# Kernel optimization log

Hardware: AMD Instinct MI355X
Metric: run time of the kernel (lower is better)

The kernel has to match this reference:

```python
import jax, jax.numpy as jnp
import numpy as np

N_NODES = 100000
N_EDGES = 3200000
IN_F, HID_F, OUT_F = 128, 128, 64
BN_EPS = 1e-5


def setup_inputs() -> dict:
    key = jax.random.key(0)
    ks = jax.random.split(key, 12)
    x = jax.random.normal(ks[0], (N_NODES, IN_F), dtype=jnp.float32)
    src = jax.random.randint(ks[1], (N_EDGES,), 0, N_NODES, dtype=jnp.int64)
    dst = jax.random.randint(ks[2], (N_EDGES,), 0, N_NODES, dtype=jnp.int64)
    s = 0.05
    W1 = jax.random.normal(ks[3], (IN_F, HID_F), dtype=jnp.float32) * s
    b1 = jnp.zeros((HID_F,), jnp.float32)
    W2 = jax.random.normal(ks[4], (HID_F, HID_F), dtype=jnp.float32) * s
    b2 = jnp.zeros((HID_F,), jnp.float32)
    W3 = jax.random.normal(ks[5], (HID_F, OUT_F), dtype=jnp.float32) * s
    b3 = jnp.zeros((OUT_F,), jnp.float32)
    gamma1 = jnp.ones((HID_F,), jnp.float32)
    beta1 = jnp.zeros((HID_F,), jnp.float32)
    gamma2 = jnp.ones((HID_F,), jnp.float32)
    beta2 = jnp.zeros((HID_F,), jnp.float32)
    return {"x": x, "src": src, "dst": dst,
            "W1": W1, "b1": b1, "W2": W2, "b2": b2, "W3": W3, "b3": b3,
            "gamma1": gamma1, "beta1": beta1, "gamma2": gamma2, "beta2": beta2}


def reference(x, src, dst, W1, b1, W2, b2, W3, b3, gamma1, beta1, gamma2, beta2):
    n = x.shape[0]
    ones = jnp.ones((src.shape[0],), x.dtype)
    # DGL GraphConv(norm='both'): symmetric normalization, degrees clamped to >=1
    deg_out = jax.ops.segment_sum(ones, src, num_segments=n)
    deg_in = jax.ops.segment_sum(ones, dst, num_segments=n)
    norm_s = jax.lax.rsqrt(jnp.maximum(deg_out, 1.0))[:, None]
    norm_d = jax.lax.rsqrt(jnp.maximum(deg_in, 1.0))[:, None]

    def conv(h, W, b):
        h = h * norm_s                                   # [N, F] scale by out-deg^{-1/2}
        m = jax.ops.segment_sum(h[src], dst, num_segments=n)  # SpMM aggregation
        return (m * norm_d) @ W + b

    def bn(h, g, b):  # BatchNorm1d, training-mode batch stats (biased var)
        mu = jnp.mean(h, axis=0)
        var = jnp.var(h, axis=0)
        return (h - mu) * jax.lax.rsqrt(var + BN_EPS) * g + b

    h = bn(jax.nn.relu(conv(x, W1, b1)), gamma1, beta1)
    h = bn(jax.nn.relu(conv(h, W2, b2)), gamma2, beta2)
    h = conv(h, W3, b3)
    return jax.nn.log_softmax(h, axis=1)
```

## Files before the change

kernel.cpp:

```cpp
#include <hip/hip_runtime.h>
#include <hip/hip_bf16.h>
#include <cstdint>

static constexpr int N = 100000;
static constexpr int E = 3200000;
static constexpr float BN_EPS = 1e-5f;
static constexpr int NBUCK = (N + 127) >> 7;
static constexpr int NBLK = 256;
static constexpr int CHUNK = E / NBLK;
static constexpr int AGG_BLOCKS = 2048;
static constexpr int NWAVE = AGG_BLOCKS * 4;

static constexpr size_t OFF_TOT_D = 0;
static constexpr size_t OFF_TOT_S = 3328;
static constexpr size_t OFF_DBASE = 6656;
static constexpr size_t OFF_SBASE = 9984;
static constexpr size_t OFF_AB1   = 13312;
static constexpr size_t OFF_AB2   = 14336;
static constexpr size_t OFF_CVEC  = 15360;
static constexpr size_t OFF_WT    = 16384;
static constexpr size_t OFF_WSRT  = 49152;
static constexpr size_t OFF_BNP2  = 82944;
static constexpr size_t OFF_BNP   = 148480;
static constexpr size_t OFF_NORM_S= 2245632;
static constexpr size_t OFF_NORM_D= 2645632;
static constexpr size_t OFF_RP    = 3045632;
static constexpr size_t OFF_CNT_D = 3445760;
static constexpr size_t OFF_CNT_S = 4246528;
static constexpr size_t OFF_OFFD  = 5047296;
static constexpr size_t OFF_OFFS  = 5848064;
static constexpr size_t OFF_COL   = 6648832;
static constexpr size_t OFF_SRCB  = 19448832;
static constexpr size_t OFF_PAIRS = 22648832;
static constexpr size_t OFF_H     = 35448832;
static constexpr size_t OFF_T     = 61048832;

using short8  = __attribute__((ext_vector_type(8))) short;
using float4v = __attribute__((ext_vector_type(4))) float;

__device__ inline float bflo(unsigned v) { return __uint_as_float(v << 16); }
__device__ inline float bfhi(unsigned v) { return __uint_as_float(v & 0xffff0000u); }
__device__ inline unsigned short bfbits(float x) {
    __hip_bfloat16 h = __float2bfloat16(x);
    return *reinterpret_cast<unsigned short*>(&h);
}

__global__ __launch_bounds__(256) void k_count(const int* __restrict__ src,
                                               const int* __restrict__ dst,
                                               int* __restrict__ cnt_s,
                                               int* __restrict__ cnt_d) {
    __shared__ int hs[NBUCK], hd[NBUCK];
    int tid = threadIdx.x, blk = blockIdx.x;
    for (int b = tid; b < NBUCK; b += 256) { hs[b] = 0; hd[b] = 0; }
    __syncthreads();
    int e0 = blk * CHUNK, e1 = min(E, e0 + CHUNK);
    for (int e = e0 + tid; e < e1; e += 256) {
        atomicAdd(&hs[src[e] >> 7], 1);
        atomicAdd(&hd[dst[e] >> 7], 1);
    }
    __syncthreads();
    for (int b = tid; b < NBUCK; b += 256) {
        cnt_s[blk * NBUCK + b] = hs[b];
        cnt_d[blk * NBUCK + b] = hd[b];
    }
}

__global__ __launch_bounds__(256) void k_scanA(const int* __restrict__ cnt,
                                               int* __restrict__ off,
                                               int* __restrict__ tot) {
    __shared__ int sd[256];
    int b = blockIdx.x, tid = threadIdx.x;
    int v = cnt[tid * NBUCK + b];
    sd[tid] = v;
    __syncthreads();
    for (int o = 1; o < 256; o <<= 1) {
        int t = (tid >= o) ? sd[tid - o] : 0;
        __syncthreads();
        sd[tid] += t;
        __syncthreads();
    }
    off[tid * NBUCK + b] = sd[tid] - v;
    if (tid == 255) tot[b] = sd[255];
}

__global__ __launch_bounds__(1024) void k_scanB(const int* __restrict__ tot_d,
                                                const int* __restrict__ tot_s,
                                                int* __restrict__ dbase,
                                                int* __restrict__ sbase) {
    __shared__ int sd[1024], ss[1024];
    int tid = threadIdx.x;
    int vd = (tid < NBUCK) ? tot_d[tid] : 0;
    int vs = (tid < NBUCK) ? tot_s[tid] : 0;
    sd[tid] = vd; ss[tid] = vs;
    __syncthreads();
    for (int o = 1; o < 1024; o <<= 1) {
        int td = (tid >= o) ? sd[tid - o] : 0;
        int ts = (tid >= o) ? ss[tid - o] : 0;
        __syncthreads();
        sd[tid] += td; ss[tid] += ts;
        __syncthreads();
    }
    if (tid < NBUCK) { dbase[tid] = sd[tid] - vd; sbase[tid] = ss[tid] - vs; }
    if (tid == 0) { dbase[NBUCK] = E; sbase[NBUCK] = E; }
}

__global__ __launch_bounds__(256) void k_scatter(const int* __restrict__ src,
                                                 const int* __restrict__ dst,
                                                 const int* __restrict__ dbase,
                                                 const int* __restrict__ sbase,
                                                 const int* __restrict__ offd,
                                                 const int* __restrict__ offs,
                                                 unsigned* __restrict__ pairs,
                                                 unsigned char* __restrict__ srcb) {
    __shared__ int cd[NBUCK], cs[NBUCK];
    int tid = threadIdx.x, blk = blockIdx.x;
    for (int b = tid; b < NBUCK; b += 256) {
        cd[b] = dbase[b] + offd[blk * NBUCK + b];
        cs[b] = sbase[b] + offs[blk * NBUCK + b];
    }
    __syncthreads();
    int e0 = blk * CHUNK, e1 = min(E, e0 + CHUNK);
    for (int e = e0 + tid; e < e1; e += 256) {
        int s = src[e], d = dst[e];
        int pd = atomicAdd(&cd[d >> 7], 1);
        pairs[pd] = (unsigned)s | ((unsigned)(d & 127) << 20);
        int ps = atomicAdd(&cs[s >> 7], 1);
        srcb[ps] = (unsigned char)(s & 127);
    }
}

__global__ __launch_bounds__(256) void k_build(const unsigned* __restrict__ pairs,
                                               const unsigned char* __restrict__ srcb,
                                               const int* __restrict__ dbase,
                                               const int* __restrict__ sbase,
                                               int* __restrict__ rp,
                                               float* __restrict__ norm_d,
                                               float* __restrict__ norm_s,
                                               int* __restrict__ col) {
    __shared__ int cnt[128], scn[128], lcur[128];
    int b = blockIdx.x, tid = threadIdx.x, node0 = b << 7;
    int nmax = min(128, N - node0);
    if (tid < 128) cnt[tid] = 0;
    __syncthreads();
    int sb = sbase[b], se = sbase[b + 1];
    for (int e = sb + tid; e < se; e += 256) atomicAdd(&cnt[srcb[e]], 1);
    __syncthreads();
    if (tid < nmax) norm_s[node0 + tid] = rsqrtf(fmaxf((float)cnt[tid], 1.0f));
    __syncthreads();
    if (tid < 128) cnt[tid] = 0;
    __syncthreads();
    int beg = dbase[b], end = dbase[b + 1];
    for (int e = beg + tid; e < end; e += 256) atomicAdd(&cnt[pairs[e] >> 20], 1);
    __syncthreads();
    if (tid < 128) scn[tid] = cnt[tid];
    __syncthreads();
    for (int o = 1; o < 128; o <<= 1) {
        int t = (tid < 128 && tid >= o) ? scn[tid - o] : 0;
        __syncthreads();
        if (tid < 128) scn[tid] += t;
        __syncthreads();
    }
    if (tid < nmax) {
        int excl = beg + scn[tid] - cnt[tid];
        rp[node0 + tid] = excl;
        lcur[tid] = excl;
        norm_d[node0 + tid] = rsqrtf(fmaxf((float)cnt[tid], 1.0f));
    }
    if (b == 0 && tid == 0) rp[N] = E;
    __syncthreads();
    for (int e = beg + tid; e < end; e += 256) {
        unsigned p = pairs[e];
        int pos = atomicAdd(&lcur[p >> 20], 1);
        col[pos] = (int)(p & 0xFFFFFu);
    }
}

__global__ __launch_bounds__(256) void k_wpart(const int* __restrict__ rp,
                                               int* __restrict__ wsrt) {
    int w = blockIdx.x * 256 + threadIdx.x;
    if (w > NWAVE) return;
    if (w == 0) { wsrt[0] = 0; return; }
    if (w == NWAVE) { wsrt[NWAVE] = N; return; }
    int t = (int)((long long)w * E / NWAVE);
    int lo = 0, hi = N;
    while (lo < hi) { int mid = (lo + hi) >> 1; if (rp[mid] >= t) hi = mid; else lo = mid + 1; }
    wsrt[w] = lo;
}

template <bool AFFINE>
__global__ __launch_bounds__(64) void k_wprep(const float* __restrict__ W,
                                              const float* __restrict__ ab,
                                              int fout,
                                              unsigned short* __restrict__ Wt,
                                              float* __restrict__ cvec) {
    int n = blockIdx.x, k = threadIdx.x;
    float w0 = W[k * fout + n], w1 = W[(k + 64) * fout + n];
    float a0 = AFFINE ? ab[k] : 1.0f;
    float a1 = AFFINE ? ab[k + 64] : 1.0f;
    Wt[n * 128 + k] = bfbits(a0 * w0);
    Wt[n * 128 + k + 64] = bfbits(a1 * w1);
    float cv = AFFINE ? (ab[128 + k] * w0 + ab[192 + k] * w1) : 0.0f;
    for (int o = 32; o; o >>= 1) cv += __shfl_xor(cv, o);
    if (k == 0) cvec[n] = cv;
}

template <typename TIn, int FOUT>
__global__ __launch_bounds__(256) void k_gemm(const TIn* __restrict__ in,
                                              const unsigned short* __restrict__ Wt,
                                              const float* __restrict__ cvec,
                                              const float* __restrict__ ns,
                                              unsigned short* __restrict__ out) {
    constexpr int PK = 72;
    __shared__ __align__(16) unsigned short Xs[128 * PK];
    __shared__ __align__(16) unsigned short Wsh[FOUT * PK];
    const int tid = threadIdx.x;
    const int r0 = blockIdx.x * 128;
    const int wave = tid >> 6, lane = tid & 63;
    const int l16 = lane & 15, quad = lane >> 4;
    constexpr int MT = (FOUT == 128) ? 4 : 2;
    constexpr int NT = 4;
    const int wm = (FOUT == 128) ? (wave >> 1) : wave;
    const int wn = (FOUT == 128) ? (wave & 1) : 0;
    const int mbase = wm * (MT * 16);
    const int nbase = wn * 64;

    float4v acc[MT][NT];
#pragma unroll
    for (int mt = 0; mt < MT; ++mt)
#pragma unroll
        for (int nt = 0; nt < NT; ++nt) acc[mt][nt] = (float4v){0.f, 0.f, 0.f, 0.f};

    for (int kb = 0; kb < 128; kb += 64) {
        __syncthreads();
        for (int i = tid; i < 128 * 8; i += 256) {
            int row = i >> 3, j = i & 7;
            int grow = r0 + row;
            if constexpr (sizeof(TIn) == 4) {
                short8 p = {0, 0, 0, 0, 0, 0, 0, 0};
                if (grow < N) {
                    const float* g = (const float*)in + (size_t)grow * 128 + kb + j * 8;
                    float4 f0 = *(const float4*)g;
                    float4 f1 = *(const float4*)(g + 4);
                    p[0] = (short)bfbits(f0.x); p[1] = (short)bfbits(f0.y);
                    p[2] = (short)bfbits(f0.z); p[3] = (short)bfbits(f0.w);
                    p[4] = (short)bfbits(f1.x); p[5] = (short)bfbits(f1.y);
                    p[6] = (short)bfbits(f1.z); p[7] = (short)bfbits(f1.w);
                }
                *(short8*)&Xs[row * PK + j * 8] = p;
            } else {
                uint4 v = make_uint4(0, 0, 0, 0);
                if (grow < N)
                    v = *(const uint4*)((const unsigned short*)in + (size_t)grow * 128 + kb + j * 8);
                *(uint4*)&Xs[row * PK + j * 8] = v;
            }
        }
        for (int i = tid; i < FOUT * 8; i += 256) {
            int n = i >> 3, j = i & 7;
            uint4 v = *(const uint4*)&Wt[n * 128 + kb + j * 8];
            *(uint4*)&Wsh[n * PK + j * 8] = v;
        }
        __syncthreads();
#pragma unroll
        for (int ks = 0; ks < 64; ks += 32) {
            short8 af[MT], bfr[NT];
#pragma unroll
            for (int mt = 0; mt < MT; ++mt)
                af[mt] = *(const short8*)&Xs[(mbase + mt * 16 + l16) * PK + ks + quad * 8];
#pragma unroll
            for (int nt = 0; nt < NT; ++nt)
                bfr[nt] = *(const short8*)&Wsh[(nbase + nt * 16 + l16) * PK + ks + quad * 8];
#pragma unroll
            for (int mt = 0; mt < MT; ++mt)
#pragma unroll
                for (int nt = 0; nt < NT; ++nt)
                    acc[mt][nt] = __builtin_amdgcn_mfma_f32_16x16x32_bf16(
                        af[mt], bfr[nt], acc[mt][nt], 0, 0, 0);
        }
    }
    float cv[NT];
#pragma unroll
    for (int nt = 0; nt < NT; ++nt) cv[nt] = cvec[nbase + nt * 16 + l16];
#pragma unroll
    for (int mt = 0; mt < MT; ++mt) {
#pragma unroll
        for (int r = 0; r < 4; ++r) {
            int row = r0 + mbase + mt * 16 + quad * 4 + r;
            if (row < N) {
                float s = ns[row];
#pragma unroll
                for (int nt = 0; nt < NT; ++nt)
                    out[(size_t)row * FOUT + nbase + nt * 16 + l16] =
                        bfbits((acc[mt][nt][r] + cv[nt]) * s);
            }
        }
    }
}

__global__ __launch_bounds__(256) void k_agg128f(const unsigned* __restrict__ T2,
                                                 const int* __restrict__ wsrt,
                                                 const int* __restrict__ rp,
                                                 const int* __restrict__ col,
                                                 const float* __restrict__ norm_d,
                                                 const float* __restrict__ bias,
                                                 unsigned* __restrict__ Hu,
                                                 float* __restrict__ part) {
    int tid = threadIdx.x, wave = tid >> 6, lane = tid & 63;
    int w = blockIdx.x * 4 + wave;
    int n0 = wsrt[w], n1 = wsrt[w + 1];
    float bb0 = bias[2 * lane], bb1 = bias[2 * lane + 1];
    float s0 = 0.f, q0 = 0.f, s1 = 0.f, q1 = 0.f;
    for (int n = n0; n < n1; ++n) {
        int beg = rp[n], end = rp[n + 1];
        float a0 = 0.0f, a1 = 0.0f;
        int e = beg;
        for (; e + 8 <= end; e += 8) {
            int c0 = col[e],     c1 = col[e + 1], c2 = col[e + 2], c3 = col[e + 3];
            int c4 = col[e + 4], c5 = col[e + 5], c6 = col[e + 6], c7 = col[e + 7];
            unsigned v0 = T2[c0 * 64 + lane];
            unsigned v1 = T2[c1 * 64 + lane];
            unsigned v2 = T2[c2 * 64 + lane];
            unsigned v3 = T2[c3 * 64 + lane];
            unsigned v4 = T2[c4 * 64 + lane];
            unsigned v5 = T2[c5 * 64 + lane];
            unsigned v6 = T2[c6 * 64 + lane];
            unsigned v7 = T2[c7 * 64 + lane];
            a0 += bflo(v0) + bflo(v1) + bflo(v2) + bflo(v3)
                + bflo(v4) + bflo(v5) + bflo(v6) + bflo(v7);
            a1 += bfhi(v0) + bfhi(v1) + bfhi(v2) + bfhi(v3)
                + bfhi(v4) + bfhi(v5) + bfhi(v6) + bfhi(v7);
        }
        for (; e < end; ++e) {
            unsigned v = T2[col[e] * 64 + lane];
            a0 += bflo(v); a1 += bfhi(v);
        }
        float nd = norm_d[n];
        float r0 = fmaxf(a0 * nd + bb0, 0.0f);
        float r1 = fmaxf(a1 * nd + bb1, 0.0f);
        Hu[n * 64 + lane] = ((unsigned)bfbits(r1) << 16) | bfbits(r0);
        s0 += r0; q0 += r0 * r0; s1 += r1; q1 += r1 * r1;
    }
    __shared__ float red[4][256];
    red[wave][lane] = s0;
    red[wave][64 + lane] = q0;
    red[wave][128 + lane] = s1;
    red[wave][192 + lane] = q1;
    __syncthreads();
    float t = red[0][tid] + red[1][tid] + red[2][tid] + red[3][tid];
    part[blockIdx.x * 256 + tid] = t;
}

__global__ __launch_bounds__(256) void k_bnred(const float* __restrict__ part,
                                               float* __restrict__ part2) {
    int b = blockIdx.x, tid = threadIdx.x;
    float s = 0.f;
    for (int i = 0; i < AGG_BLOCKS / 64; ++i)
        s += part[(b * (AGG_BLOCKS / 64) + i) * 256 + tid];
    part2[b * 256 + tid] = s;
}

__global__ __launch_bounds__(256) void k_bnfin(const float* __restrict__ part2,
                                               const float* __restrict__ gamma,
                                               const float* __restrict__ beta,
                                               float* __restrict__ ab) {
    __shared__ float slot[256];
    int tid = threadIdx.x;
    float a = 0.f;
    for (int b = 0; b < 64; ++b) a += part2[b * 256 + tid];
    slot[tid] = a;
    __syncthreads();
    if (tid < 128) {
        int l = tid >> 1;
        float sum, sq;
        if ((tid & 1) == 0) { sum = slot[l];       sq = slot[64 + l]; }
        else                { sum = slot[128 + l]; sq = slot[192 + l]; }
        float mu = sum * (1.0f / N);
        float var = sq * (1.0f / N) - mu * mu;
        float aa = gamma[tid] * rsqrtf(var + BN_EPS);
        ab[tid] = aa;
        ab[128 + tid] = beta[tid] - mu * aa;
    }
}

__global__ __launch_bounds__(256) void k_agg64f(const __hip_bfloat16* __restrict__ T,
                                                const int* __restrict__ wsrt,
                                                const int* __restrict__ rp,
                                                const int* __restrict__ col,
                                                const float* __restrict__ norm_d,
                                                const float* __restrict__ b3,
                                                float* __restrict__ out) {
    int wave = threadIdx.x >> 6, lane = threadIdx.x & 63;
    int w = blockIdx.x * 4 + wave;
    int n0 = wsrt[w], n1 = wsrt[w + 1];
    float bb = b3[lane];
    for (int n = n0; n < n1; ++n) {
        int beg = rp[n], end = rp[n + 1];
        float a0 = 0.0f;
        int e = beg;
        for (; e + 8 <= end; e += 8) {
            int c0 = col[e],     c1 = col[e + 1], c2 = col[e + 2], c3 = col[e + 3];
            int c4 = col[e + 4], c5 = col[e + 5], c6 = col[e + 6], c7 = col[e + 7];
            float v0 = __bfloat162float(T[c0 * 64 + lane]);
            float v1 = __bfloat162float(T[c1 * 64 + lane]);
            float v2 = __bfloat162float(T[c2 * 64 + lane]);
            float v3 = __bfloat162float(T[c3 * 64 + lane]);
            float v4 = __bfloat162float(T[c4 * 64 + lane]);
            float v5 = __bfloat162float(T[c5 * 64 + lane]);
            float v6 = __bfloat162float(T[c6 * 64 + lane]);
            float v7 = __bfloat162float(T[c7 * 64 + lane]);
            a0 += v0 + v1 + v2 + v3 + v4 + v5 + v6 + v7;
        }
        for (; e < end; ++e) a0 += __bfloat162float(T[col[e] * 64 + lane]);
        float z = a0 * norm_d[n] + bb;
        float m = z;
        for (int off = 32; off; off >>= 1) m = fmaxf(m, __shfl_xor(m, off));
        float ex = __expf(z - m);
        float ssum = ex;
        for (int off = 32; off; off >>= 1) ssum += __shfl_xor(ssum, off);
        out[n * 64 + lane] = z - m - __logf(ssum);
    }
}

extern "C" void kernel_launch(void* const* d_in, const int* in_sizes, int n_in,
                              void* d_out, int out_size, void* d_ws, size_t ws_size,
                              hipStream_t stream) {
    const float* x  = (const float*)d_in[0];
    const int* src  = (const int*)d_in[1];
    const int* dst  = (const int*)d_in[2];
    const float* W1 = (const float*)d_in[3];
    const float* b1 = (const float*)d_in[4];
    const float* W2 = (const float*)d_in[5];
    const float* b2 = (const float*)d_in[6];
    const float* W3 = (const float*)d_in[7];
    const float* b3 = (const float*)d_in[8];
    const float* g1 = (const float*)d_in[9];
    const float* be1= (const float*)d_in[10];
    const float* g2 = (const float*)d_in[11];
    const float* be2= (const float*)d_in[12];
    float* out = (float*)d_out;

    char* ws = (char*)d_ws;
    int* tot_d = (int*)(ws + OFF_TOT_D);
    int* tot_s = (int*)(ws + OFF_TOT_S);
    int* dbase = (int*)(ws + OFF_DBASE);
    int* sbase = (int*)(ws + OFF_SBASE);
    float* ab1 = (float*)(ws + OFF_AB1);
    float* ab2 = (float*)(ws + OFF_AB2);
    float* cvec = (float*)(ws + OFF_CVEC);
    unsigned short* Wt = (unsigned short*)(ws + OFF_WT);
    int* wsrt = (int*)(ws + OFF_WSRT);
    float* bnp2 = (float*)(ws + OFF_BNP2);
    float* bnp = (float*)(ws + OFF_BNP);
    float* norm_s = (float*)(ws + OFF_NORM_S);
    float* norm_d = (float*)(ws + OFF_NORM_D);
    int* rp = (int*)(ws + OFF_RP);
    int* cnt_d = (int*)(ws + OFF_CNT_D);
    int* cnt_s = (int*)(ws + OFF_CNT_S);
    int* offd = (int*)(ws + OFF_OFFD);
    int* offs = (int*)(ws + OFF_OFFS);
    int* col = (int*)(ws + OFF_COL);
    unsigned char* srcb = (unsigned char*)(ws + OFF_SRCB);
    unsigned* pairs = (unsigned*)(ws + OFF_PAIRS);
    unsigned short* H = (unsigned short*)(ws + OFF_H);
    unsigned short* T = (unsigned short*)(ws + OFF_T);

    k_count<<<NBLK, 256, 0, stream>>>(src, dst, cnt_s, cnt_d);
    k_scanA<<<NBUCK, 256, 0, stream>>>(cnt_d, offd, tot_d);
    k_scanA<<<NBUCK, 256, 0, stream>>>(cnt_s, offs, tot_s);
    k_scanB<<<1, 1024, 0, stream>>>(tot_d, tot_s, dbase, sbase);
    k_scatter<<<NBLK, 256, 0, stream>>>(src, dst, dbase, sbase, offd, offs, pairs, srcb);
    k_build<<<NBUCK, 256, 0, stream>>>(pairs, srcb, dbase, sbase, rp, norm_d, norm_s, col);
    k_wpart<<<(NWAVE + 256) / 256, 256, 0, stream>>>(rp, wsrt);

    const int gemm_grid = (N + 127) / 128;

    k_wprep<false><<<128, 64, 0, stream>>>(W1, nullptr, 128, Wt, cvec);
    k_gemm<float, 128><<<gemm_grid, 256, 0, stream>>>(x, Wt, cvec, norm_s, T);
    k_agg128f<<<AGG_BLOCKS, 256, 0, stream>>>((const unsigned*)T, wsrt, rp, col, norm_d, b1, (unsigned*)H, bnp);
    k_bnred<<<64, 256, 0, stream>>>(bnp, bnp2);
    k_bnfin<<<1, 256, 0, stream>>>(bnp2, g1, be1, ab1);

    k_wprep<true><<<128, 64, 0, stream>>>(W2, ab1, 128, Wt, cvec);
    k_gemm<__hip_bfloat16, 128><<<gemm_grid, 256, 0, stream>>>((const __hip_bfloat16*)H, Wt, cvec, norm_s, T);
    k_agg128f<<<AGG_BLOCKS, 256, 0, stream>>>((const unsigned*)T, wsrt, rp, col, norm_d, b2, (unsigned*)H, bnp);
    k_bnred<<<64, 256, 0, stream>>>(bnp, bnp2);
    k_bnfin<<<1, 256, 0, stream>>>(bnp2, g2, be2, ab2);

    k_wprep<true><<<64, 64, 0, stream>>>(W3, ab2, 64, Wt, cvec);
    k_gemm<__hip_bfloat16, 64><<<gemm_grid, 256, 0, stream>>>((const __hip_bfloat16*)H, Wt, cvec, norm_s, T);
    k_agg64f<<<AGG_BLOCKS, 256, 0, stream>>>((const __hip_bfloat16*)T, wsrt, rp, col, norm_d, b3, out);
}
```

Measured before the change: 656.0 us.

## Slice feature matrices into column panels for cache-local sparse aggregation

The intermediate T and H buffers are stored as column-sliced panels (8 slices of 16 bf16 features per node), and aggregation blocks are assigned to one slice each, so the gathered working set per slice is a fraction of the full matrix and can stay resident in cache. Within a wave, lanes are split between edges and features, then combined with cross-lane shuffles, so each wave processes several edges at once. The final layer writes pre-softmax logits to a scratch buffer and runs log-softmax in a separate kernel, and the BN partial reductions are reorganised per slice. In exchange the col indices and rp are re-read once per slice, and the extra shuffle reductions and extra kernel add overhead.

```diff
diff --git a/kernel.cpp b/kernel.cpp
--- a/kernel.cpp
+++ b/kernel.cpp
@@ -8,8 +8,9 @@
 static constexpr int NBUCK = (N + 127) >> 7;
 static constexpr int NBLK = 256;
 static constexpr int CHUNK = E / NBLK;
-static constexpr int AGG_BLOCKS = 2048;
-static constexpr int NWAVE = AGG_BLOCKS * 4;
+static constexpr int PARTS = 256;
+static constexpr int AGG_BLOCKS = PARTS * 8;
+static constexpr int NWAVE = PARTS * 4;
 
 static constexpr size_t OFF_TOT_D = 0;
 static constexpr size_t OFF_TOT_S = 3328;
@@ -34,6 +35,7 @@
 static constexpr size_t OFF_PAIRS = 22648832;
 static constexpr size_t OFF_H     = 35448832;
 static constexpr size_t OFF_T     = 61048832;
+static constexpr size_t OFF_Z     = 86648832;
 
 using short8  = __attribute__((ext_vector_type(8))) short;
 using float4v = __attribute__((ext_vector_type(4))) float;
@@ -249,8 +251,12 @@
                 *(short8*)&Xs[row * PK + j * 8] = p;
             } else {
                 uint4 v = make_uint4(0, 0, 0, 0);
-                if (grow < N)
-                    v = *(const uint4*)((const unsigned short*)in + (size_t)grow * 128 + kb + j * 8);
+                if (grow < N) {
+                    int ub = (kb >> 1) + j * 4;
+                    const unsigned* Hu = (const unsigned*)in;
+                    v = *(const uint4*)&Hu[(size_t)(ub >> 3) * ((size_t)N * 8)
+                                           + (size_t)grow * 8 + (ub & 7)];
+                }
                 *(uint4*)&Xs[row * PK + j * 8] = v;
             }
         }
@@ -288,15 +294,20 @@
             if (row < N) {
                 float s = ns[row];
 #pragma unroll
-                for (int nt = 0; nt < NT; ++nt)
-                    out[(size_t)row * FOUT + nbase + nt * 16 + l16] =
-                        bfbits((acc[mt][nt][r] + cv[nt]) * s);
+                for (int nt = 0; nt < NT; ++nt) {
+                    int f = nbase + nt * 16 + l16;
+                    unsigned short val = bfbits((acc[mt][nt][r] + cv[nt]) * s);
+                    if (FOUT == 128)
+                        out[(size_t)(f >> 4) * ((size_t)N * 16) + (size_t)row * 16 + (f & 15)] = val;
+                    else
+                        out[(size_t)(f >> 3) * ((size_t)N * 8) + (size_t)row * 8 + (f & 7)] = val;
+                }
             }
         }
     }
 }
 
-__global__ __launch_bounds__(256) void k_agg128f(const unsigned* __restrict__ T2,
+__global__ __launch_bounds__(256) void k_agg128s(const unsigned* __restrict__ Tu,
                                                  const int* __restrict__ wsrt,
                                                  const int* __restrict__ rp,
                                                  const int* __restrict__ col,
@@ -305,119 +316,146 @@
                                                  unsigned* __restrict__ Hu,
                                                  float* __restrict__ part) {
     int tid = threadIdx.x, wave = tid >> 6, lane = tid & 63;
-    int w = blockIdx.x * 4 + wave;
+    int slice = blockIdx.x & 7, prt = blockIdx.x >> 3;
+    int w = prt * 4 + wave;
     int n0 = wsrt[w], n1 = wsrt[w + 1];
-    float bb0 = bias[2 * lane], bb1 = bias[2 * lane + 1];
+    int le = lane >> 3, lu = lane & 7;
+    const unsigned* Ts = Tu + (size_t)slice * ((size_t)N * 8);
+    unsigned* Hs = Hu + (size_t)slice * ((size_t)N * 8);
+    float bb0 = bias[slice * 16 + lu * 2];
+    float bb1 = bias[slice * 16 + lu * 2 + 1];
     float s0 = 0.f, q0 = 0.f, s1 = 0.f, q1 = 0.f;
     for (int n = n0; n < n1; ++n) {
         int beg = rp[n], end = rp[n + 1];
-        float a0 = 0.0f, a1 = 0.0f;
+        float a0 = 0.f, a1 = 0.f;
         int e = beg;
+        for (; e + 32 <= end; e += 32) {
+            int c0 = col[e + le], c1 = col[e + 8 + le];
+            int c2 = col[e + 16 + le], c3 = col[e + 24 + le];
+            unsigned v0 = Ts[c0 * 8 + lu];
+            unsigned v1 = Ts[c1 * 8 + lu];
+            unsigned v2 = Ts[c2 * 8 + lu];
+            unsigned v3 = Ts[c3 * 8 + lu];
+            a0 += bflo(v0) + bflo(v1) + bflo(v2) + bflo(v3);
+            a1 += bfhi(v0) + bfhi(v1) + bfhi(v2) + bfhi(v3);
+        }
         for (; e + 8 <= end; e += 8) {
-            int c0 = col[e],     c1 = col[e + 1], c2 = col[e + 2], c3 = col[e + 3];
-            int c4 = col[e + 4], c5 = col[e + 5], c6 = col[e + 6], c7 = col[e + 7];
-            unsigned v0 = T2[c0 * 64 + lane];
-            unsigned v1 = T2[c1 * 64 + lane];
-            unsigned v2 = T2[c2 * 64 + lane];
-            unsigned v3 = T2[c3 * 64 + lane];
-            unsigned v4 = T2[c4 * 64 + lane];
-            unsigned v5 = T2[c5 * 64 + lane];
-            unsigned v6 = T2[c6 * 64 + lane];
-            unsigned v7 = T2[c7 * 64 + lane];
-            a0 += bflo(v0) + bflo(v1) + bflo(v2) + bflo(v3)
-                + bflo(v4) + bflo(v5) + bflo(v6) + bflo(v7);
-            a1 += bfhi(v0) + bfhi(v1) + bfhi(v2) + bfhi(v3)
-                + bfhi(v4) + bfhi(v5) + bfhi(v6) + bfhi(v7);
-        }
-        for (; e < end; ++e) {
-            unsigned v = T2[col[e] * 64 + lane];
+            unsigned v = Ts[col[e + le] * 8 + lu];
             a0 += bflo(v); a1 += bfhi(v);
         }
+        if (e + le < end) {
+            unsigned v = Ts[col[e + le] * 8 + lu];
+            a0 += bflo(v); a1 += bfhi(v);
+        }
+        a0 += __shfl_xor(a0, 8);  a1 += __shfl_xor(a1, 8);
+        a0 += __shfl_xor(a0, 16); a1 += __shfl_xor(a1, 16);
+        a0 += __shfl_xor(a0, 32); a1 += __shfl_xor(a1, 32);
         float nd = norm_d[n];
-        float r0 = fmaxf(a0 * nd + bb0, 0.0f);
-        float r1 = fmaxf(a1 * nd + bb1, 0.0f);
-        Hu[n * 64 + lane] = ((unsigned)bfbits(r1) << 16) | bfbits(r0);
+        float r0 = fmaxf(a0 * nd + bb0, 0.f);
+        float r1 = fmaxf(a1 * nd + bb1, 0.f);
+        if (lane < 8) Hs[n * 8 + lu] = ((unsigned)bfbits(r1) << 16) | bfbits(r0);
         s0 += r0; q0 += r0 * r0; s1 += r1; q1 += r1 * r1;
     }
-    __shared__ float red[4][256];
-    red[wave][lane] = s0;
-    red[wave][64 + lane] = q0;
-    red[wave][128 + lane] = s1;
-    red[wave][192 + lane] = q1;
-    __syncthreads();
-    float t = red[0][tid] + red[1][tid] + red[2][tid] + red[3][tid];
-    part[blockIdx.x * 256 + tid] = t;
-}
-
-__global__ __launch_bounds__(256) void k_bnred(const float* __restrict__ part,
-                                               float* __restrict__ part2) {
-    int b = blockIdx.x, tid = threadIdx.x;
+    __shared__ float red[4][32];
+    if (lane < 8) {
+        red[wave][lu * 4 + 0] = s0;
+        red[wave][lu * 4 + 1] = q0;
+        red[wave][lu * 4 + 2] = s1;
+        red[wave][lu * 4 + 3] = q1;
+    }
+    __syncthreads();
+    if (tid < 32)
+        part[blockIdx.x * 32 + tid] = red[0][tid] + red[1][tid] + red[2][tid] + red[3][tid];
+}
+
+__global__ __launch_bounds__(64) void k_bnred(const float* __restrict__ part,
+                                              float* __restrict__ part2) {
+    int g = blockIdx.x, tid = threadIdx.x;
+    if (tid >= 32) return;
+    int slice = g & 7, chunk = g >> 3;
     float s = 0.f;
-    for (int i = 0; i < AGG_BLOCKS / 64; ++i)
-        s += part[(b * (AGG_BLOCKS / 64) + i) * 256 + tid];
-    part2[b * 256 + tid] = s;
-}
-
-__global__ __launch_bounds__(256) void k_bnfin(const float* __restrict__ part2,
+    for (int i = 0; i < 32; ++i) {
+        int b = (chunk * 32 + i) * 8 + slice;
+        s += part[b * 32 + tid];
+    }
+    part2[g * 32 + tid] = s;
+}
+
+__global__ __launch_bounds__(128) void k_bnfin(const float* __restrict__ part2,
                                                const float* __restrict__ gamma,
                                                const float* __restrict__ beta,
                                                float* __restrict__ ab) {
-    __shared__ float slot[256];
-    int tid = threadIdx.x;
-    float a = 0.f;
-    for (int b = 0; b < 64; ++b) a += part2[b * 256 + tid];
-    slot[tid] = a;
-    __syncthreads();
-    if (tid < 128) {
-        int l = tid >> 1;
-        float sum, sq;
-        if ((tid & 1) == 0) { sum = slot[l];       sq = slot[64 + l]; }
-        else                { sum = slot[128 + l]; sq = slot[192 + l]; }
-        float mu = sum * (1.0f / N);
-        float var = sq * (1.0f / N) - mu * mu;
-        float aa = gamma[tid] * rsqrtf(var + BN_EPS);
-        ab[tid] = aa;
-        ab[128 + tid] = beta[tid] - mu * aa;
-    }
-}
-
-__global__ __launch_bounds__(256) void k_agg64f(const __hip_bfloat16* __restrict__ T,
+    int f = threadIdx.x;
+    int slice = f >> 4, lu = (f & 15) >> 1, par = f & 1;
+    float s = 0.f, q = 0.f;
+    for (int chunk = 0; chunk < 8; ++chunk) {
+        int g = chunk * 8 + slice;
+        s += part2[g * 32 + lu * 4 + par * 2 + 0];
+        q += part2[g * 32 + lu * 4 + par * 2 + 1];
+    }
+    float mu = s * (1.0f / N);
+    float var = q * (1.0f / N) - mu * mu;
+    float aa = gamma[f] * rsqrtf(var + BN_EPS);
+    ab[f] = aa;
+    ab[128 + f] = beta[f] - mu * aa;
+}
+
+__global__ __launch_bounds__(256) void k_agg64s(const unsigned* __restrict__ Tu,
                                                 const int* __restrict__ wsrt,
                                                 const int* __restrict__ rp,
                                                 const int* __restrict__ col,
                                                 const float* __restrict__ norm_d,
                                                 const float* __restrict__ b3,
-                                                float* __restrict__ out) {
-    int wave = threadIdx.x >> 6, lane = threadIdx.x & 63;
-    int w = blockIdx.x * 4 + wave;
+                                                float* __restrict__ Z) {
+    int tid = threadIdx.x, wave = tid >> 6, lane = tid & 63;
+    int slice = blockIdx.x & 7, prt = blockIdx.x >> 3;
+    int w = prt * 4 + wave;
     int n0 = wsrt[w], n1 = wsrt[w + 1];
-    float bb = b3[lane];
+    int le = lane >> 2, lu = lane & 3;
+    const unsigned* Ts = Tu + (size_t)slice * ((size_t)N * 4);
+    float bb0 = b3[slice * 8 + lu * 2], bb1 = b3[slice * 8 + lu * 2 + 1];
     for (int n = n0; n < n1; ++n) {
         int beg = rp[n], end = rp[n + 1];
-        float a0 = 0.0f;
+        float a0 = 0.f, a1 = 0.f;
         int e = beg;
-        for (; e + 8 <= end; e += 8) {
-            int c0 = col[e],     c1 = col[e + 1], c2 = col[e + 2], c3 = col[e + 3];
-            int c4 = col[e + 4], c5 = col[e + 5], c6 = col[e + 6], c7 = col[e + 7];
-            float v0 = __bfloat162float(T[c0 * 64 + lane]);
-            float v1 = __bfloat162float(T[c1 * 64 + lane]);
-            float v2 = __bfloat162float(T[c2 * 64 + lane]);
-            float v3 = __bfloat162float(T[c3 * 64 + lane]);
-            float v4 = __bfloat162float(T[c4 * 64 + lane]);
-            float v5 = __bfloat162float(T[c5 * 64 + lane]);
-            float v6 = __bfloat162float(T[c6 * 64 + lane]);
-            float v7 = __bfloat162float(T[c7 * 64 + lane]);
-            a0 += v0 + v1 + v2 + v3 + v4 + v5 + v6 + v7;
-        }
-        for (; e < end; ++e) a0 += __bfloat162float(T[col[e] * 64 + lane]);
-        float z = a0 * norm_d[n] + bb;
-        float m = z;
-        for (int off = 32; off; off >>= 1) m = fmaxf(m, __shfl_xor(m, off));
-        float ex = __expf(z - m);
-        float ssum = ex;
-        for (int off = 32; off; off >>= 1) ssum += __shfl_xor(ssum, off);
-        out[n * 64 + lane] = z - m - __logf(ssum);
-    }
+        for (; e + 32 <= end; e += 32) {
+            int c0 = col[e + le], c1 = col[e + 16 + le];
+            unsigned v0 = Ts[c0 * 4 + lu], v1 = Ts[c1 * 4 + lu];
+            a0 += bflo(v0) + bflo(v1);
+            a1 += bfhi(v0) + bfhi(v1);
+        }
+        for (; e + 16 <= end; e += 16) {
+            unsigned v = Ts[col[e + le] * 4 + lu];
+            a0 += bflo(v); a1 += bfhi(v);
+        }
+        if (e + le < end) {
+            unsigned v = Ts[col[e + le] * 4 + lu];
+            a0 += bflo(v); a1 += bfhi(v);
+        }
+        a0 += __shfl_xor(a0, 4);  a1 += __shfl_xor(a1, 4);
+        a0 += __shfl_xor(a0, 8);  a1 += __shfl_xor(a1, 8);
+        a0 += __shfl_xor(a0, 16); a1 += __shfl_xor(a1, 16);
+        a0 += __shfl_xor(a0, 32); a1 += __shfl_xor(a1, 32);
+        float nd = norm_d[n];
+        if (lane < 4) {
+            float2 z = make_float2(a0 * nd + bb0, a1 * nd + bb1);
+            *(float2*)&Z[(size_t)n * 64 + slice * 8 + lu * 2] = z;
+        }
+    }
+}
+
+__global__ __launch_bounds__(256) void k_lsm(const float* __restrict__ Z,
+                                             float* __restrict__ out) {
+    int wave = threadIdx.x >> 6, lane = threadIdx.x & 63;
+    int n = blockIdx.x * 4 + wave;
+    if (n >= N) return;
+    float z = Z[(size_t)n * 64 + lane];
+    float m = z;
+    for (int o = 32; o; o >>= 1) m = fmaxf(m, __shfl_xor(m, o));
+    float ex = __expf(z - m);
+    float ss = ex;
+    for (int o = 32; o; o >>= 1) ss += __shfl_xor(ss, o);
+    out[(size_t)n * 64 + lane] = z - m - __logf(ss);
 }
 
 extern "C" void kernel_launch(void* const* d_in, const int* in_sizes, int n_in,
@@ -462,6 +500,7 @@
     unsigned* pairs = (unsigned*)(ws + OFF_PAIRS);
     unsigned short* H = (unsigned short*)(ws + OFF_H);
     unsigned short* T = (unsigned short*)(ws + OFF_T);
+    float* Z = (float*)(ws + OFF_Z);
 
     k_count<<<NBLK, 256, 0, stream>>>(src, dst, cnt_s, cnt_d);
     k_scanA<<<NBUCK, 256, 0, stream>>>(cnt_d, offd, tot_d);
@@ -475,17 +514,18 @@
 
     k_wprep<false><<<128, 64, 0, stream>>>(W1, nullptr, 128, Wt, cvec);
     k_gemm<float, 128><<<gemm_grid, 256, 0, stream>>>(x, Wt, cvec, norm_s, T);
-    k_agg128f<<<AGG_BLOCKS, 256, 0, stream>>>((const unsigned*)T, wsrt, rp, col, norm_d, b1, (unsigned*)H, bnp);
-    k_bnred<<<64, 256, 0, stream>>>(bnp, bnp2);
-    k_bnfin<<<1, 256, 0, stream>>>(bnp2, g1, be1, ab1);
+    k_agg128s<<<AGG_BLOCKS, 256, 0, stream>>>((const unsigned*)T, wsrt, rp, col, norm_d, b1, (unsigned*)H, bnp);
+    k_bnred<<<64, 64, 0, stream>>>(bnp, bnp2);
+    k_bnfin<<<1, 128, 0, stream>>>(bnp2, g1, be1, ab1);
 
     k_wprep<true><<<128, 64, 0, stream>>>(W2, ab1, 128, Wt, cvec);
-    k_gemm<__hip_bfloat16, 128><<<gemm_grid, 256, 0, stream>>>((const __hip_bfloat16*)H, Wt, cvec, norm_s, T);
-    k_agg128f<<<AGG_BLOCKS, 256, 0, stream>>>((const unsigned*)T, wsrt, rp, col, norm_d, b2, (unsigned*)H, bnp);
-    k_bnred<<<64, 256, 0, stream>>>(bnp, bnp2);
-    k_bnfin<<<1, 256, 0, stream>>>(bnp2, g2, be2, ab2);
+    k_gemm<unsigned short, 128><<<gemm_grid, 256, 0, stream>>>(H, Wt, cvec, norm_s, T);
+    k_agg128s<<<AGG_BLOCKS, 256, 0, stream>>>((const unsigned*)T, wsrt, rp, col, norm_d, b2, (unsigned*)H, bnp);
+    k_bnred<<<64, 64, 0, stream>>>(bnp, bnp2);
+    k_bnfin<<<1, 128, 0, stream>>>(bnp2, g2, be2, ab2);
 
     k_wprep<true><<<64, 64, 0, stream>>>(W3, ab2, 64, Wt, cvec);
-    k_gemm<__hip_bfloat16, 64><<<gemm_grid, 256, 0, stream>>>((const __hip_bfloat16*)H, Wt, cvec, norm_s, T);
-    k_agg64f<<<AGG_BLOCKS, 256, 0, stream>>>((const __hip_bfloat16*)T, wsrt, rp, col, norm_d, b3, out);
-}
+    k_gemm<unsigned short, 64><<<gemm_grid, 256, 0, stream>>>(H, Wt, cvec, norm_s, T);
+    k_agg64s<<<AGG_BLOCKS, 256, 0, stream>>>((const unsigned*)T, wsrt, rp, col, norm_d, b3, Z);
+    k_lsm<<<(N + 3) / 4, 256, 0, stream>>>(Z, out);
+}
```

Result: slower. 1.049 ms (+59.8%).

## Widen SpMM gathers to 8-byte loads with multiple edges per wave

Applied to the files above, without the earlier changes.

The aggregation kernels now load uint2 (4 bf16 features) per lane. Half-waves (128-wide) or quarter-waves (64-wide) each handle a different edge, and partial sums are combined with cross-lane shuffles. The goal is to cut gather instruction count and issue more independent row fetches per wave. The BN statistics layout and the bnfin reduction are reworked to match the new per-lane feature mapping. In exchange, extra shuffles and only partial-lane stores are added.

```diff
diff --git a/kernel.cpp b/kernel.cpp
--- a/kernel.cpp
+++ b/kernel.cpp
@@ -296,56 +296,76 @@
     }
 }
 
-__global__ __launch_bounds__(256) void k_agg128f(const unsigned* __restrict__ T2,
+__global__ __launch_bounds__(256) void k_agg128f(const uint2* __restrict__ T2,
                                                  const int* __restrict__ wsrt,
                                                  const int* __restrict__ rp,
                                                  const int* __restrict__ col,
                                                  const float* __restrict__ norm_d,
                                                  const float* __restrict__ bias,
-                                                 unsigned* __restrict__ Hu,
+                                                 uint2* __restrict__ Hu,
                                                  float* __restrict__ part) {
     int tid = threadIdx.x, wave = tid >> 6, lane = tid & 63;
+    int le = lane >> 5, lu = lane & 31;
     int w = blockIdx.x * 4 + wave;
     int n0 = wsrt[w], n1 = wsrt[w + 1];
-    float bb0 = bias[2 * lane], bb1 = bias[2 * lane + 1];
+    float bb0 = bias[4 * lu], bb1 = bias[4 * lu + 1];
+    float bb2 = bias[4 * lu + 2], bb3 = bias[4 * lu + 3];
     float s0 = 0.f, q0 = 0.f, s1 = 0.f, q1 = 0.f;
+    float s2 = 0.f, q2 = 0.f, s3 = 0.f, q3 = 0.f;
     for (int n = n0; n < n1; ++n) {
         int beg = rp[n], end = rp[n + 1];
-        float a0 = 0.0f, a1 = 0.0f;
+        float a0 = 0.f, a1 = 0.f, a2 = 0.f, a3 = 0.f;
         int e = beg;
-        for (; e + 8 <= end; e += 8) {
-            int c0 = col[e],     c1 = col[e + 1], c2 = col[e + 2], c3 = col[e + 3];
-            int c4 = col[e + 4], c5 = col[e + 5], c6 = col[e + 6], c7 = col[e + 7];
-            unsigned v0 = T2[c0 * 64 + lane];
-            unsigned v1 = T2[c1 * 64 + lane];
-            unsigned v2 = T2[c2 * 64 + lane];
-            unsigned v3 = T2[c3 * 64 + lane];
-            unsigned v4 = T2[c4 * 64 + lane];
-            unsigned v5 = T2[c5 * 64 + lane];
-            unsigned v6 = T2[c6 * 64 + lane];
-            unsigned v7 = T2[c7 * 64 + lane];
-            a0 += bflo(v0) + bflo(v1) + bflo(v2) + bflo(v3)
-                + bflo(v4) + bflo(v5) + bflo(v6) + bflo(v7);
-            a1 += bfhi(v0) + bfhi(v1) + bfhi(v2) + bfhi(v3)
-                + bfhi(v4) + bfhi(v5) + bfhi(v6) + bfhi(v7);
-        }
-        for (; e < end; ++e) {
-            unsigned v = T2[col[e] * 64 + lane];
-            a0 += bflo(v); a1 += bfhi(v);
-        }
+        for (; e + 16 <= end; e += 16) {
+            uint2 v[8];
+#pragma unroll
+            for (int i = 0; i < 8; ++i) {
+                int cA = col[e + 2 * i], cB = col[e + 2 * i + 1];
+                int c = le ? cB : cA;
+                v[i] = T2[(size_t)c * 32 + lu];
+            }
+#pragma unroll
+            for (int i = 0; i < 8; ++i) {
+                a0 += bflo(v[i].x); a1 += bfhi(v[i].x);
+                a2 += bflo(v[i].y); a3 += bfhi(v[i].y);
+            }
+        }
+        for (; e + 2 <= end; e += 2) {
+            int cA = col[e], cB = col[e + 1];
+            int c = le ? cB : cA;
+            uint2 v = T2[(size_t)c * 32 + lu];
+            a0 += bflo(v.x); a1 += bfhi(v.x);
+            a2 += bflo(v.y); a3 += bfhi(v.y);
+        }
+        if (e < end && le == 0) {
+            uint2 v = T2[(size_t)col[e] * 32 + lu];
+            a0 += bflo(v.x); a1 += bfhi(v.x);
+            a2 += bflo(v.y); a3 += bfhi(v.y);
+        }
+        a0 += __shfl_xor(a0, 32); a1 += __shfl_xor(a1, 32);
+        a2 += __shfl_xor(a2, 32); a3 += __shfl_xor(a3, 32);
         float nd = norm_d[n];
-        float r0 = fmaxf(a0 * nd + bb0, 0.0f);
-        float r1 = fmaxf(a1 * nd + bb1, 0.0f);
-        Hu[n * 64 + lane] = ((unsigned)bfbits(r1) << 16) | bfbits(r0);
+        float r0 = fmaxf(a0 * nd + bb0, 0.f), r1 = fmaxf(a1 * nd + bb1, 0.f);
+        float r2 = fmaxf(a2 * nd + bb2, 0.f), r3 = fmaxf(a3 * nd + bb3, 0.f);
+        if (le == 0) {
+            uint2 hv;
+            hv.x = ((unsigned)bfbits(r1) << 16) | bfbits(r0);
+            hv.y = ((unsigned)bfbits(r3) << 16) | bfbits(r2);
+            Hu[(size_t)n * 32 + lu] = hv;
+        }
         s0 += r0; q0 += r0 * r0; s1 += r1; q1 += r1 * r1;
-    }
-    __shared__ float red[4][256];
-    red[wave][lane] = s0;
-    red[wave][64 + lane] = q0;
-    red[wave][128 + lane] = s1;
-    red[wave][192 + lane] = q1;
-    __syncthreads();
-    float t = red[0][tid] + red[1][tid] + red[2][tid] + red[3][tid];
+        s2 += r2; q2 += r2 * r2; s3 += r3; q3 += r3 * r3;
+    }
+    __shared__ float red[4][32][8];
+    if (le == 0) {
+        red[wave][lu][0] = s0; red[wave][lu][1] = q0;
+        red[wave][lu][2] = s1; red[wave][lu][3] = q1;
+        red[wave][lu][4] = s2; red[wave][lu][5] = q2;
+        red[wave][lu][6] = s3; red[wave][lu][7] = q3;
+    }
+    __syncthreads();
+    float t = red[0][tid >> 3][tid & 7] + red[1][tid >> 3][tid & 7]
+            + red[2][tid >> 3][tid & 7] + red[3][tid >> 3][tid & 7];
     part[blockIdx.x * 256 + tid] = t;
 }
 
@@ -358,30 +378,25 @@
     part2[b * 256 + tid] = s;
 }
 
-__global__ __launch_bounds__(256) void k_bnfin(const float* __restrict__ part2,
+__global__ __launch_bounds__(128) void k_bnfin(const float* __restrict__ part2,
                                                const float* __restrict__ gamma,
                                                const float* __restrict__ beta,
                                                float* __restrict__ ab) {
-    __shared__ float slot[256];
-    int tid = threadIdx.x;
-    float a = 0.f;
-    for (int b = 0; b < 64; ++b) a += part2[b * 256 + tid];
-    slot[tid] = a;
-    __syncthreads();
-    if (tid < 128) {
-        int l = tid >> 1;
-        float sum, sq;
-        if ((tid & 1) == 0) { sum = slot[l];       sq = slot[64 + l]; }
-        else                { sum = slot[128 + l]; sq = slot[192 + l]; }
-        float mu = sum * (1.0f / N);
-        float var = sq * (1.0f / N) - mu * mu;
-        float aa = gamma[tid] * rsqrtf(var + BN_EPS);
-        ab[tid] = aa;
-        ab[128 + tid] = beta[tid] - mu * aa;
-    }
-}
-
-__global__ __launch_bounds__(256) void k_agg64f(const __hip_bfloat16* __restrict__ T,
+    int f = threadIdx.x;
+    int lu = f >> 2, c = f & 3;
+    float s = 0.f, q = 0.f;
+    for (int b = 0; b < 64; ++b) {
+        s += part2[b * 256 + lu * 8 + c * 2];
+        q += part2[b * 256 + lu * 8 + c * 2 + 1];
+    }
+    float mu = s * (1.0f / N);
+    float var = q * (1.0f / N) - mu * mu;
+    float aa = gamma[f] * rsqrtf(var + BN_EPS);
+    ab[f] = aa;
+    ab[128 + f] = beta[f] - mu * aa;
+}
+
+__global__ __launch_bounds__(256) void k_agg64f(const uint2* __restrict__ T2,
                                                 const int* __restrict__ wsrt,
                                                 const int* __restrict__ rp,
                                                 const int* __restrict__ col,
@@ -389,34 +404,68 @@
                                                 const float* __restrict__ b3,
                                                 float* __restrict__ out) {
     int wave = threadIdx.x >> 6, lane = threadIdx.x & 63;
+    int le = lane >> 4, lu = lane & 15;
     int w = blockIdx.x * 4 + wave;
     int n0 = wsrt[w], n1 = wsrt[w + 1];
-    float bb = b3[lane];
+    float bb0 = b3[4 * lu], bb1 = b3[4 * lu + 1];
+    float bb2 = b3[4 * lu + 2], bb3 = b3[4 * lu + 3];
     for (int n = n0; n < n1; ++n) {
         int beg = rp[n], end = rp[n + 1];
-        float a0 = 0.0f;
+        float a0 = 0.f, a1 = 0.f, a2 = 0.f, a3 = 0.f;
         int e = beg;
-        for (; e + 8 <= end; e += 8) {
-            int c0 = col[e],     c1 = col[e + 1], c2 = col[e + 2], c3 = col[e + 3];
-            int c4 = col[e + 4], c5 = col[e + 5], c6 = col[e + 6], c7 = col[e + 7];
-            float v0 = __bfloat162float(T[c0 * 64 + lane]);
-            float v1 = __bfloat162float(T[c1 * 64 + lane]);
-            float v2 = __bfloat162float(T[c2 * 64 + lane]);
-            float v3 = __bfloat162float(T[c3 * 64 + lane]);
-            float v4 = __bfloat162float(T[c4 * 64 + lane]);
-            float v5 = __bfloat162float(T[c5 * 64 + lane]);
-            float v6 = __bfloat162float(T[c6 * 64 + lane]);
-            float v7 = __bfloat162float(T[c7 * 64 + lane]);
-            a0 += v0 + v1 + v2 + v3 + v4 + v5 + v6 + v7;
-        }
-        for (; e < end; ++e) a0 += __bfloat162float(T[col[e] * 64 + lane]);
-        float z = a0 * norm_d[n] + bb;
-        float m = z;
-        for (int off = 32; off; off >>= 1) m = fmaxf(m, __shfl_xor(m, off));
-        float ex = __expf(z - m);
-        float ssum = ex;
-        for (int off = 32; off; off >>= 1) ssum += __shfl_xor(ssum, off);
-        out[n * 64 + lane] = z - m - __logf(ssum);
+        for (; e + 32 <= end; e += 32) {
+            uint2 v[8];
+#pragma unroll
+            for (int i = 0; i < 8; ++i) {
+                int cA = col[e + 4 * i], cB = col[e + 4 * i + 1];
+                int cC = col[e + 4 * i + 2], cD = col[e + 4 * i + 3];
+                int c01 = (le & 1) ? cB : cA;
+                int c23 = (le & 1) ? cD : cC;
+                int c = (le & 2) ? c23 : c01;
+                v[i] = T2[(size_t)c * 16 + lu];
+            }
+#pragma unroll
+            for (int i = 0; i < 8; ++i) {
+                a0 += bflo(v[i].x); a1 += bfhi(v[i].x);
+                a2 += bflo(v[i].y); a3 += bfhi(v[i].y);
+            }
+        }
+        for (; e + 4 <= end; e += 4) {
+            int cA = col[e], cB = col[e + 1], cC = col[e + 2], cD = col[e + 3];
+            int c01 = (le & 1) ? cB : cA;
+            int c23 = (le & 1) ? cD : cC;
+            int c = (le & 2) ? c23 : c01;
+            uint2 v = T2[(size_t)c * 16 + lu];
+            a0 += bflo(v.x); a1 += bfhi(v.x);
+            a2 += bflo(v.y); a3 += bfhi(v.y);
+        }
+        if (e + le < end) {
+            uint2 v = T2[(size_t)col[e + le] * 16 + lu];
+            a0 += bflo(v.x); a1 += bfhi(v.x);
+            a2 += bflo(v.y); a3 += bfhi(v.y);
+        }
+        a0 += __shfl_xor(a0, 16); a1 += __shfl_xor(a1, 16);
+        a2 += __shfl_xor(a2, 16); a3 += __shfl_xor(a3, 16);
+        a0 += __shfl_xor(a0, 32); a1 += __shfl_xor(a1, 32);
+        a2 += __shfl_xor(a2, 32); a3 += __shfl_xor(a3, 32);
+        float nd = norm_d[n];
+        float z0 = a0 * nd + bb0, z1 = a1 * nd + bb1;
+        float z2 = a2 * nd + bb2, z3 = a3 * nd + bb3;
+        float m = fmaxf(fmaxf(z0, z1), fmaxf(z2, z3));
+        m = fmaxf(m, __shfl_xor(m, 1));
+        m = fmaxf(m, __shfl_xor(m, 2));
+        m = fmaxf(m, __shfl_xor(m, 4));
+        m = fmaxf(m, __shfl_xor(m, 8));
+        float ex = __expf(z0 - m) + __expf(z1 - m) + __expf(z2 - m) + __expf(z3 - m);
+        ex += __shfl_xor(ex, 1);
+        ex += __shfl_xor(ex, 2);
+        ex += __shfl_xor(ex, 4);
+        ex += __shfl_xor(ex, 8);
+        float l = m + __logf(ex);
+        if (le == 0) {
+            float4 o4 = make_float4(z0 - l, z1 - l, z2 - l, z3 - l);
+            *(float4*)&out[(size_t)n * 64 + lu * 4] = o4;
+        }
     }
 }
 
@@ -475,17 +524,17 @@
 
     k_wprep<false><<<128, 64, 0, stream>>>(W1, nullptr, 128, Wt, cvec);
     k_gemm<float, 128><<<gemm_grid, 256, 0, stream>>>(x, Wt, cvec, norm_s, T);
-    k_agg128f<<<AGG_BLOCKS, 256, 0, stream>>>((const unsigned*)T, wsrt, rp, col, norm_d, b1, (unsigned*)H, bnp);
+    k_agg128f<<<AGG_BLOCKS, 256, 0, stream>>>((const uint2*)T, wsrt, rp, col, norm_d, b1, (uint2*)H, bnp);
     k_bnred<<<64, 256, 0, stream>>>(bnp, bnp2);
-    k_bnfin<<<1, 256, 0, stream>>>(bnp2, g1, be1, ab1);
+    k_bnfin<<<1, 128, 0, stream>>>(bnp2, g1, be1, ab1);
 
     k_wprep<true><<<128, 64, 0, stream>>>(W2, ab1, 128, Wt, cvec);
     k_gemm<__hip_bfloat16, 128><<<gemm_grid, 256, 0, stream>>>((const __hip_bfloat16*)H, Wt, cvec, norm_s, T);
-    k_agg128f<<<AGG_BLOCKS, 256, 0, stream>>>((const unsigned*)T, wsrt, rp, col, norm_d, b2, (unsigned*)H, bnp);
+    k_agg128f<<<AGG_BLOCKS, 256, 0, stream>>>((const uint2*)T, wsrt, rp, col, norm_d, b2, (uint2*)H, bnp);
     k_bnred<<<64, 256, 0, stream>>>(bnp, bnp2);
-    k_bnfin<<<1, 256, 0, stream>>>(bnp2, g2, be2, ab2);
+    k_bnfin<<<1, 128, 0, stream>>>(bnp2, g2, be2, ab2);
 
     k_wprep<true><<<64, 64, 0, stream>>>(W3, ab2, 64, Wt, cvec);
     k_gemm<__hip_bfloat16, 64><<<gemm_grid, 256, 0, stream>>>((const __hip_bfloat16*)H, Wt, cvec, norm_s, T);
-    k_agg64f<<<AGG_BLOCKS, 256, 0, stream>>>((const __hip_bfloat16*)T, wsrt, rp, col, norm_d, b3, out);
-}
+    k_agg64f<<<AGG_BLOCKS, 256, 0, stream>>>((const uint2*)T, wsrt, rp, col, norm_d, b3, out);
+}
```

After: 724.1 us. +10.4%, slower.
